# Kernel optimization log

Hardware: AMD Instinct MI355X
Metric: run time of the kernel (lower is better)

## Reference

```python
import jax, jax.numpy as jnp
import numpy as np

N = 8192
F_IN = 128
F_OUT = 128
NEG_SLOPE = 0.2


def setup_inputs() -> dict:
    key = jax.random.key(0)
    k_h, k_adj, k_W, k_a = jax.random.split(key, 4)
    h = jax.random.normal(k_h, (N, F_IN), dtype=jnp.float32)
    # binary adjacency mask as float (the module multiplies scores by adj)
    adj = (jax.random.uniform(k_adj, (N, N)) < 0.05).astype(jnp.float32)
    # nn.Linear(in, out, bias=False): weight shape [out, in]
    W = jax.random.normal(k_W, (F_OUT, F_IN), dtype=jnp.float32) / np.sqrt(F_IN)
    # nn.Linear(2*out, 1, bias=False): weight shape [1, 2*out]
    a = jax.random.normal(k_a, (1, 2 * F_OUT), dtype=jnp.float32) / np.sqrt(2 * F_OUT)
    return {"h": h, "adj": adj, "W": W, "a": a}


def reference(h, adj, W, a):
    # Wh: [N, F_out]
    Wh = h @ W.T
    f = Wh.shape[-1]
    # a([Wh_i ; Wh_j]) factored: e[i, j] = leaky_relu(Wh[i]@a1 + Wh[j]@a2)
    a1 = a[0, :f]  # [F_out]
    a2 = a[0, f:]  # [F_out]
    s_i = Wh @ a1  # [N]
    s_j = Wh @ a2  # [N]
    e = jax.nn.leaky_relu(s_i[:, None] + s_j[None, :], NEG_SLOPE)  # [N, N]
    # faithful to original: softmax over dim=1 of e * adj (multiplicative mask)
    attention = jax.nn.softmax(e * adj, axis=1)  # [N, N]
    return attention @ Wh  # [N, F_out]
```

## Files before the change

kernel.cpp:

```cpp
#include <hip/hip_runtime.h>

#define N_NODES 8192
#define FDIM 128
#define NEG_SLOPE 0.2f
#define SEG 512

__device__ __forceinline__ unsigned int f2bf(float f) {
  unsigned int u = __float_as_uint(f);
  return (u + 0x7FFFu + ((u >> 16) & 1u)) >> 16;
}

__global__ __launch_bounds__(256) void transpose_w_kernel(
    const float* __restrict__ W, float* __restrict__ WtG) {
  int idx = blockIdx.x * 256 + threadIdx.x;
  WtG[idx] = W[(idx & 127) * FDIM + (idx >> 7)];
}

__global__ __launch_bounds__(256) void wh_fused_kernel(
    const float* __restrict__ h, const float* __restrict__ WtG,
    const float* __restrict__ a,
    unsigned int* __restrict__ Whb,
    float* __restrict__ s1, float* __restrict__ s2,
    float* __restrict__ S) {
  __shared__ float Wt[FDIM * 132];
  __shared__ float rows[32 * 132];
  const int t = threadIdx.x;
  const int base = blockIdx.x * 32;
  for (int it = 0; it < 16; ++it) {
    int idx = t + 256 * it;
    int k = idx >> 5, c = (idx & 31) * 4;
    *(float4*)&Wt[k * 132 + c] = *(const float4*)&WtG[k * FDIM + c];
  }
  for (int it = 0; it < 4; ++it) {
    int idx = t + 256 * it;
    int r = idx >> 5, c = (idx & 31) * 4;
    *(float4*)&rows[r * 132 + c] =
        *(const float4*)&h[(size_t)(base + r) * FDIM + c];
  }
  __syncthreads();
  const int c4 = (t & 31) * 4;
  const int g = t >> 5;
  float acc[4][4];
#pragma unroll
  for (int rr = 0; rr < 4; ++rr)
#pragma unroll
    for (int cc = 0; cc < 4; ++cc) acc[rr][cc] = 0.f;
  for (int k = 0; k < FDIM; ++k) {
    float4 wv = *(const float4*)&Wt[k * 132 + c4];
    float rv[4];
#pragma unroll
    for (int rr = 0; rr < 4; ++rr) rv[rr] = rows[(4 * g + rr) * 132 + k];
#pragma unroll
    for (int rr = 0; rr < 4; ++rr) {
      acc[rr][0] += rv[rr] * wv.x;
      acc[rr][1] += rv[rr] * wv.y;
      acc[rr][2] += rv[rr] * wv.z;
      acc[rr][3] += rv[rr] * wv.w;
    }
  }
#pragma unroll
  for (int rr = 0; rr < 4; ++rr) {
    int r = base + 4 * g + rr;
    unsigned int p0 = f2bf(acc[rr][0]) | (f2bf(acc[rr][1]) << 16);
    unsigned int p1 = f2bf(acc[rr][2]) | (f2bf(acc[rr][3]) << 16);
    *(uint2*)&Whb[(size_t)r * 64 + (c4 >> 1)] = make_uint2(p0, p1);
  }
  {
    float4 a1v = *(const float4*)&a[c4];
    float4 a2v = *(const float4*)&a[FDIM + c4];
#pragma unroll
    for (int rr = 0; rr < 4; ++rr) {
      float d1 = acc[rr][0] * a1v.x + acc[rr][1] * a1v.y +
                 acc[rr][2] * a1v.z + acc[rr][3] * a1v.w;
      float d2 = acc[rr][0] * a2v.x + acc[rr][1] * a2v.y +
                 acc[rr][2] * a2v.z + acc[rr][3] * a2v.w;
#pragma unroll
      for (int off = 16; off; off >>= 1) {
        d1 += __shfl_down(d1, off);
        d2 += __shfl_down(d2, off);
      }
      if ((t & 31) == 0) {
        s1[base + 4 * g + rr] = d1;
        s2[base + 4 * g + rr] = d2;
      }
    }
  }
  __syncthreads();
  float4 cs = make_float4(acc[0][0] + acc[1][0] + acc[2][0] + acc[3][0],
                          acc[0][1] + acc[1][1] + acc[2][1] + acc[3][1],
                          acc[0][2] + acc[1][2] + acc[2][2] + acc[3][2],
                          acc[0][3] + acc[1][3] + acc[2][3] + acc[3][3]);
  *(float4*)&rows[g * FDIM + c4] = cs;
  __syncthreads();
  if (t < FDIM) {
    float s = 0.f;
#pragma unroll
    for (int gg = 0; gg < 8; ++gg) s += rows[gg * FDIM + t];
    atomicAdd(&S[t], s);
  }
}

__device__ __forceinline__ float4 ntload4(const float4* p) {
  typedef float f4v __attribute__((ext_vector_type(4)));
  f4v v = __builtin_nontemporal_load((const f4v*)p);
  return make_float4(v[0], v[1], v[2], v[3]);
}

__device__ __forceinline__ int mbcnt64(unsigned long long b) {
  return (int)__builtin_amdgcn_mbcnt_hi(
      (unsigned)(b >> 32), __builtin_amdgcn_mbcnt_lo((unsigned)b, 0u));
}

__global__ __launch_bounds__(256, 4) void gat_row_kernel(
    const float* __restrict__ adj, const unsigned int* __restrict__ Whb,
    const float* __restrict__ s1, const float* __restrict__ s2,
    const float* __restrict__ S, float* __restrict__ out) {
  const int i = blockIdx.x;
  const int t = threadIdx.x;
  const int lane = t & 63;
  const int wave = t >> 6;
  __shared__ float2 pairs[4 * SEG];
  __shared__ int counts[4];
  __shared__ float red[4];
  __shared__ float red2[4];
  __shared__ float fpart[4][FDIM];

  const float s1i = s1[i];
  const float4* __restrict__ arow = (const float4*)(adj + (size_t)i * N_NODES);
  const float4* __restrict__ srow = (const float4*)s2;
  float2* __restrict__ mypairs = pairs + wave * SEG;

  float4 av[8], sv[8];
#pragma unroll
  for (int it = 0; it < 8; ++it) av[it] = ntload4(&arow[it * 256 + t]);
#pragma unroll
  for (int it = 0; it < 8; ++it) sv[it] = srow[it * 256 + t];
  int cbase = 0;
  float lmax = -1e30f;
#pragma unroll
  for (int it = 0; it < 8; ++it) {
    const int j4 = it * 256 + t;
    float vv[4] = {av[it].x, av[it].y, av[it].z, av[it].w};
    float ss[4] = {sv[it].x, sv[it].y, sv[it].z, sv[it].w};
#pragma unroll
    for (int c = 0; c < 4; ++c) {
      bool pred = (vv[c] != 0.f);
      float e = s1i + ss[c];
      e = e > 0.f ? e : NEG_SLOPE * e;
      unsigned long long b = __ballot(pred);
      if (pred) {
        int pos = cbase + mbcnt64(b);
        if (pos < SEG) {
          float2 pr;
          pr.x = e;
          ((int*)&pr)[1] = j4 * 4 + c;
          mypairs[pos] = pr;
        }
      }
      lmax = fmaxf(lmax, pred ? e : -1e30f);
      cbase += (int)__popcll(b);
    }
  }
  const int mycnt = cbase < SEG ? cbase : SEG;
  if (lane == 0) counts[wave] = mycnt;
  for (int off = 32; off; off >>= 1) lmax = fmaxf(lmax, __shfl_down(lmax, off));
  if (lane == 0) red[wave] = lmax;
  __syncthreads();
  const int cnt = counts[0] + counts[1] + counts[2] + counts[3];
  float m = fmaxf(fmaxf(red[0], red[1]), fmaxf(red[2], red[3]));
  if (cnt < N_NODES) m = fmaxf(m, 0.f);
  const float em = __expf(-m);

  const int half = lane >> 5, lq = lane & 31;
  const uint2* __restrict__ Whb2 = (const uint2*)Whb;
  float ax = 0.f, ay = 0.f, az = 0.f, aw = 0.f, lsum = 0.f;
  const int nit = (mycnt + 1) >> 1;
  int it = 0;
  for (; it + 3 < nit; it += 4) {
#pragma unroll
    for (int c = 0; c < 4; ++c) {
      int p = 2 * (it + c) + half;
      bool ok = p < mycnt;
      float2 pr = mypairs[ok ? p : 0];
      int j = ((const int*)&pr)[1];
      uint2 d = Whb2[((size_t)j << 5) + lq];
      float pv = __expf(pr.x - m);
      float w = ok ? pv - em : 0.f;
      lsum += ok ? pv : 0.f;
      ax += w * __uint_as_float(d.x << 16);
      ay += w * __uint_as_float(d.x & 0xffff0000u);
      az += w * __uint_as_float(d.y << 16);
      aw += w * __uint_as_float(d.y & 0xffff0000u);
    }
  }
  for (; it < nit; ++it) {
    int p = 2 * it + half;
    bool ok = p < mycnt;
    float2 pr = mypairs[ok ? p : 0];
    int j = ((const int*)&pr)[1];
    uint2 d = Whb2[((size_t)j << 5) + lq];
    float pv = __expf(pr.x - m);
    float w = ok ? pv - em : 0.f;
    lsum += ok ? pv : 0.f;
    ax += w * __uint_as_float(d.x << 16);
    ay += w * __uint_as_float(d.x & 0xffff0000u);
    az += w * __uint_as_float(d.y << 16);
    aw += w * __uint_as_float(d.y & 0xffff0000u);
  }
  for (int off = 32; off; off >>= 1) lsum += __shfl_down(lsum, off);
  if (lane == 0) red2[wave] = lsum * (1.f / 32.f);
  ax += __shfl_down(ax, 32);
  ay += __shfl_down(ay, 32);
  az += __shfl_down(az, 32);
  aw += __shfl_down(aw, 32);
  if (lane < 32)
    *(float4*)&fpart[wave][4 * lq] = make_float4(ax, ay, az, aw);
  __syncthreads();
  if (t < FDIM) {
    float l = red2[0] + red2[1] + red2[2] + red2[3]
              + (float)(N_NODES - cnt) * em;
    float o = (fpart[0][t] + fpart[1][t] + fpart[2][t] + fpart[3][t]
               + em * S[t]) / l;
    out[(size_t)i * FDIM + t] = o;
  }
}

extern "C" void kernel_launch(void* const* d_in, const int* in_sizes, int n_in,
                              void* d_out, int out_size, void* d_ws, size_t ws_size,
                              hipStream_t stream) {
  const float* h   = (const float*)d_in[0];
  const float* adj = (const float*)d_in[1];
  const float* W   = (const float*)d_in[2];
  const float* a   = (const float*)d_in[3];
  float* out = (float*)d_out;
  unsigned int* Whb = (unsigned int*)d_ws;
  float* s1  = (float*)(Whb + (size_t)N_NODES * 64);
  float* s2  = s1 + N_NODES;
  float* S   = s2 + N_NODES;
  float* WtG = S + FDIM;

  hipMemsetAsync(S, 0, FDIM * sizeof(float), stream);
  hipLaunchKernelGGL(transpose_w_kernel, dim3(FDIM * FDIM / 256), dim3(256), 0,
                     stream, W, WtG);
  hipLaunchKernelGGL(wh_fused_kernel, dim3(N_NODES / 32), dim3(256), 0, stream,
                     h, WtG, a, Whb, s1, s2, S);
  hipLaunchKernelGGL(gat_row_kernel, dim3(N_NODES), dim3(256), 0, stream,
                     adj, Whb, s1, s2, S, out);
}
```

Before: 410.2 us.

## Split row kernel into separate adjacency scan and sparse gather kernels

The fused per-row kernel is split into a scan kernel, which streams the adjacency row and writes compacted (score, index) pairs plus per-wave counts and maxima to global workspace, and a gather kernel, which reads those pairs and accumulates bf16 Wh rows. The gather now loads 16-byte vectors per lane, with four neighbours per wave step instead of two. The aim is to keep the bandwidth-bound scan from being stalled by latency-bound gathers and to let each phase run at its own occupancy. The cost is a global round trip for the pair lists (about 128 MB written and read) and an extra launch.

Measured after the change: 458.6 us. +11.8%, slower.

```diff
diff --git a/kernel.cpp b/kernel.cpp
--- a/kernel.cpp
+++ b/kernel.cpp
@@ -111,24 +111,17 @@
       (unsigned)(b >> 32), __builtin_amdgcn_mbcnt_lo((unsigned)b, 0u));
 }
 
-__global__ __launch_bounds__(256, 4) void gat_row_kernel(
-    const float* __restrict__ adj, const unsigned int* __restrict__ Whb,
-    const float* __restrict__ s1, const float* __restrict__ s2,
-    const float* __restrict__ S, float* __restrict__ out) {
+__global__ __launch_bounds__(256, 4) void scan_kernel(
+    const float* __restrict__ adj, const float* __restrict__ s1,
+    const float* __restrict__ s2, float2* __restrict__ pairs,
+    int* __restrict__ cnt4, float* __restrict__ wmax) {
   const int i = blockIdx.x;
   const int t = threadIdx.x;
-  const int lane = t & 63;
-  const int wave = t >> 6;
-  __shared__ float2 pairs[4 * SEG];
-  __shared__ int counts[4];
-  __shared__ float red[4];
-  __shared__ float red2[4];
-  __shared__ float fpart[4][FDIM];
-
+  const int lane = t & 63, wave = t >> 6;
   const float s1i = s1[i];
   const float4* __restrict__ arow = (const float4*)(adj + (size_t)i * N_NODES);
   const float4* __restrict__ srow = (const float4*)s2;
-  float2* __restrict__ mypairs = pairs + wave * SEG;
+  float2* __restrict__ mypairs = pairs + (size_t)i * (4 * SEG) + wave * SEG;
 
   float4 av[8], sv[8];
 #pragma unroll
@@ -162,59 +155,68 @@
     }
   }
   const int mycnt = cbase < SEG ? cbase : SEG;
-  if (lane == 0) counts[wave] = mycnt;
   for (int off = 32; off; off >>= 1) lmax = fmaxf(lmax, __shfl_down(lmax, off));
-  if (lane == 0) red[wave] = lmax;
-  __syncthreads();
-  const int cnt = counts[0] + counts[1] + counts[2] + counts[3];
-  float m = fmaxf(fmaxf(red[0], red[1]), fmaxf(red[2], red[3]));
+  if (lane == 0) {
+    cnt4[4 * i + wave] = mycnt;
+    wmax[4 * i + wave] = lmax;
+  }
+}
+
+__global__ __launch_bounds__(256, 4) void gather_kernel(
+    const unsigned int* __restrict__ Whb, const float2* __restrict__ pairs,
+    const int* __restrict__ cnt4, const float* __restrict__ wmax,
+    const float* __restrict__ S, float* __restrict__ out) {
+  const int i = blockIdx.x;
+  const int t = threadIdx.x;
+  const int lane = t & 63, wave = t >> 6;
+  __shared__ float fpart[4][FDIM];
+  __shared__ float red2[4];
+
+  const int4 cc = *(const int4*)&cnt4[4 * i];
+  const float4 wm = *(const float4*)&wmax[4 * i];
+  const int cnt = cc.x + cc.y + cc.z + cc.w;
+  const int mycnt = wave == 0 ? cc.x : wave == 1 ? cc.y : wave == 2 ? cc.z : cc.w;
+  float m = fmaxf(fmaxf(wm.x, wm.y), fmaxf(wm.z, wm.w));
   if (cnt < N_NODES) m = fmaxf(m, 0.f);
   const float em = __expf(-m);
 
-  const int half = lane >> 5, lq = lane & 31;
-  const uint2* __restrict__ Whb2 = (const uint2*)Whb;
-  float ax = 0.f, ay = 0.f, az = 0.f, aw = 0.f, lsum = 0.f;
-  const int nit = (mycnt + 1) >> 1;
-  int it = 0;
-  for (; it + 3 < nit; it += 4) {
-#pragma unroll
-    for (int c = 0; c < 4; ++c) {
-      int p = 2 * (it + c) + half;
-      bool ok = p < mycnt;
-      float2 pr = mypairs[ok ? p : 0];
-      int j = ((const int*)&pr)[1];
-      uint2 d = Whb2[((size_t)j << 5) + lq];
-      float pv = __expf(pr.x - m);
-      float w = ok ? pv - em : 0.f;
-      lsum += ok ? pv : 0.f;
-      ax += w * __uint_as_float(d.x << 16);
-      ay += w * __uint_as_float(d.x & 0xffff0000u);
-      az += w * __uint_as_float(d.y << 16);
-      aw += w * __uint_as_float(d.y & 0xffff0000u);
-    }
-  }
-  for (; it < nit; ++it) {
-    int p = 2 * it + half;
+  const float2* __restrict__ mypairs = pairs + (size_t)i * (4 * SEG) + wave * SEG;
+  const int q = lane >> 4, lq = lane & 15;
+  const uint4* __restrict__ Whb4 = (const uint4*)Whb;
+  float acc[8];
+#pragma unroll
+  for (int e = 0; e < 8; ++e) acc[e] = 0.f;
+  float lsum = 0.f;
+  const int nit = (mycnt + 3) >> 2;
+  for (int it = 0; it < nit; ++it) {
+    int p = 4 * it + q;
     bool ok = p < mycnt;
     float2 pr = mypairs[ok ? p : 0];
-    int j = ((const int*)&pr)[1];
-    uint2 d = Whb2[((size_t)j << 5) + lq];
+    int j = ((const int*)&pr)[1] & (N_NODES - 1);
+    uint4 d = Whb4[((size_t)j << 4) + lq];
     float pv = __expf(pr.x - m);
     float w = ok ? pv - em : 0.f;
     lsum += ok ? pv : 0.f;
-    ax += w * __uint_as_float(d.x << 16);
-    ay += w * __uint_as_float(d.x & 0xffff0000u);
-    az += w * __uint_as_float(d.y << 16);
-    aw += w * __uint_as_float(d.y & 0xffff0000u);
+    acc[0] += w * __uint_as_float(d.x << 16);
+    acc[1] += w * __uint_as_float(d.x & 0xffff0000u);
+    acc[2] += w * __uint_as_float(d.y << 16);
+    acc[3] += w * __uint_as_float(d.y & 0xffff0000u);
+    acc[4] += w * __uint_as_float(d.z << 16);
+    acc[5] += w * __uint_as_float(d.z & 0xffff0000u);
+    acc[6] += w * __uint_as_float(d.w << 16);
+    acc[7] += w * __uint_as_float(d.w & 0xffff0000u);
   }
   for (int off = 32; off; off >>= 1) lsum += __shfl_down(lsum, off);
-  if (lane == 0) red2[wave] = lsum * (1.f / 32.f);
-  ax += __shfl_down(ax, 32);
-  ay += __shfl_down(ay, 32);
-  az += __shfl_down(az, 32);
-  aw += __shfl_down(aw, 32);
-  if (lane < 32)
-    *(float4*)&fpart[wave][4 * lq] = make_float4(ax, ay, az, aw);
+  if (lane == 0) red2[wave] = lsum * (1.f / 16.f);
+#pragma unroll
+  for (int e = 0; e < 8; ++e) {
+    acc[e] += __shfl_down(acc[e], 32);
+    acc[e] += __shfl_down(acc[e], 16);
+  }
+  if (lane < 16) {
+    *(float4*)&fpart[wave][lq * 8] = make_float4(acc[0], acc[1], acc[2], acc[3]);
+    *(float4*)&fpart[wave][lq * 8 + 4] = make_float4(acc[4], acc[5], acc[6], acc[7]);
+  }
   __syncthreads();
   if (t < FDIM) {
     float l = red2[0] + red2[1] + red2[2] + red2[3]
@@ -234,16 +236,21 @@
   const float* a   = (const float*)d_in[3];
   float* out = (float*)d_out;
   unsigned int* Whb = (unsigned int*)d_ws;
-  float* s1  = (float*)(Whb + (size_t)N_NODES * 64);
-  float* s2  = s1 + N_NODES;
-  float* S   = s2 + N_NODES;
-  float* WtG = S + FDIM;
+  float* s1   = (float*)(Whb + (size_t)N_NODES * 64);
+  float* s2   = s1 + N_NODES;
+  float* S    = s2 + N_NODES;
+  float* WtG  = S + FDIM;
+  int*   cnt4 = (int*)(WtG + FDIM * FDIM);
+  float* wmax = (float*)(cnt4 + 4 * N_NODES);
+  float2* pairs = (float2*)(wmax + 4 * N_NODES);
 
   hipMemsetAsync(S, 0, FDIM * sizeof(float), stream);
   hipLaunchKernelGGL(transpose_w_kernel, dim3(FDIM * FDIM / 256), dim3(256), 0,
                      stream, W, WtG);
   hipLaunchKernelGGL(wh_fused_kernel, dim3(N_NODES / 32), dim3(256), 0, stream,
                      h, WtG, a, Whb, s1, s2, S);
-  hipLaunchKernelGGL(gat_row_kernel, dim3(N_NODES), dim3(256), 0, stream,
-                     adj, Whb, s1, s2, S, out);
-}
+  hipLaunchKernelGGL(scan_kernel, dim3(N_NODES), dim3(256), 0, stream,
+                     adj, s1, s2, pairs, cnt4, wmax);
+  hipLaunchKernelGGL(gather_kernel, dim3(N_NODES), dim3(256), 0, stream,
+                     Whb, pairs, cnt4, wmax, S, out);
+}
```

## Process four rows per block with double-buffered adjacency prefetch and wider Wh gathers

Applied to the files above, without the earlier changes.

Each block now handles four consecutive rows and issues the nontemporal adjacency loads for the next row before the current row's sync and gather phase, so the memory stream overlaps with compute. The gather phase switches from 64-bit loads over two half-waves to 128-bit loads, with four lanes groups of 16 per wave each covering one neighbour. The aim is to hide adjacency-load latency and reduce gather instructions, at the cost of more registers for the double buffer, fewer blocks, and an extra shuffle stage in the reduction. Loop-carried dependencies between rows and the shared-memory reuse across rows are guarded by the existing syncs.

Result: no change. 417.2 us (+1.7%).

```diff
diff --git a/kernel.cpp b/kernel.cpp
--- a/kernel.cpp
+++ b/kernel.cpp
@@ -4,6 +4,7 @@
 #define FDIM 128
 #define NEG_SLOPE 0.2f
 #define SEG 512
+#define ROWS 4
 
 __device__ __forceinline__ unsigned int f2bf(float f) {
   unsigned int u = __float_as_uint(f);
@@ -111,118 +112,128 @@
       (unsigned)(b >> 32), __builtin_amdgcn_mbcnt_lo((unsigned)b, 0u));
 }
 
-__global__ __launch_bounds__(256, 4) void gat_row_kernel(
+__global__ __launch_bounds__(256, 4) void gat_pipe_kernel(
     const float* __restrict__ adj, const unsigned int* __restrict__ Whb,
     const float* __restrict__ s1, const float* __restrict__ s2,
     const float* __restrict__ S, float* __restrict__ out) {
-  const int i = blockIdx.x;
   const int t = threadIdx.x;
-  const int lane = t & 63;
-  const int wave = t >> 6;
+  const int lane = t & 63, wave = t >> 6;
   __shared__ float2 pairs[4 * SEG];
   __shared__ int counts[4];
   __shared__ float red[4];
   __shared__ float red2[4];
   __shared__ float fpart[4][FDIM];
-
-  const float s1i = s1[i];
-  const float4* __restrict__ arow = (const float4*)(adj + (size_t)i * N_NODES);
+  float2* __restrict__ mypairs = pairs + wave * SEG;
   const float4* __restrict__ srow = (const float4*)s2;
-  float2* __restrict__ mypairs = pairs + wave * SEG;
-
-  float4 av[8], sv[8];
-#pragma unroll
-  for (int it = 0; it < 8; ++it) av[it] = ntload4(&arow[it * 256 + t]);
-#pragma unroll
-  for (int it = 0; it < 8; ++it) sv[it] = srow[it * 256 + t];
-  int cbase = 0;
-  float lmax = -1e30f;
-#pragma unroll
-  for (int it = 0; it < 8; ++it) {
-    const int j4 = it * 256 + t;
-    float vv[4] = {av[it].x, av[it].y, av[it].z, av[it].w};
-    float ss[4] = {sv[it].x, sv[it].y, sv[it].z, sv[it].w};
-#pragma unroll
-    for (int c = 0; c < 4; ++c) {
-      bool pred = (vv[c] != 0.f);
-      float e = s1i + ss[c];
-      e = e > 0.f ? e : NEG_SLOPE * e;
-      unsigned long long b = __ballot(pred);
-      if (pred) {
-        int pos = cbase + mbcnt64(b);
-        if (pos < SEG) {
-          float2 pr;
-          pr.x = e;
-          ((int*)&pr)[1] = j4 * 4 + c;
-          mypairs[pos] = pr;
-        }
-      }
-      lmax = fmaxf(lmax, pred ? e : -1e30f);
-      cbase += (int)__popcll(b);
-    }
-  }
-  const int mycnt = cbase < SEG ? cbase : SEG;
-  if (lane == 0) counts[wave] = mycnt;
-  for (int off = 32; off; off >>= 1) lmax = fmaxf(lmax, __shfl_down(lmax, off));
-  if (lane == 0) red[wave] = lmax;
-  __syncthreads();
-  const int cnt = counts[0] + counts[1] + counts[2] + counts[3];
-  float m = fmaxf(fmaxf(red[0], red[1]), fmaxf(red[2], red[3]));
-  if (cnt < N_NODES) m = fmaxf(m, 0.f);
-  const float em = __expf(-m);
-
-  const int half = lane >> 5, lq = lane & 31;
-  const uint2* __restrict__ Whb2 = (const uint2*)Whb;
-  float ax = 0.f, ay = 0.f, az = 0.f, aw = 0.f, lsum = 0.f;
-  const int nit = (mycnt + 1) >> 1;
-  int it = 0;
-  for (; it + 3 < nit; it += 4) {
-#pragma unroll
-    for (int c = 0; c < 4; ++c) {
-      int p = 2 * (it + c) + half;
-      bool ok = p < mycnt;
-      float2 pr = mypairs[ok ? p : 0];
-      int j = ((const int*)&pr)[1];
-      uint2 d = Whb2[((size_t)j << 5) + lq];
-      float pv = __expf(pr.x - m);
-      float w = ok ? pv - em : 0.f;
-      lsum += ok ? pv : 0.f;
-      ax += w * __uint_as_float(d.x << 16);
-      ay += w * __uint_as_float(d.x & 0xffff0000u);
-      az += w * __uint_as_float(d.y << 16);
-      aw += w * __uint_as_float(d.y & 0xffff0000u);
-    }
-  }
-  for (; it < nit; ++it) {
-    int p = 2 * it + half;
-    bool ok = p < mycnt;
-    float2 pr = mypairs[ok ? p : 0];
-    int j = ((const int*)&pr)[1];
-    uint2 d = Whb2[((size_t)j << 5) + lq];
-    float pv = __expf(pr.x - m);
-    float w = ok ? pv - em : 0.f;
-    lsum += ok ? pv : 0.f;
-    ax += w * __uint_as_float(d.x << 16);
-    ay += w * __uint_as_float(d.x & 0xffff0000u);
-    az += w * __uint_as_float(d.y << 16);
-    aw += w * __uint_as_float(d.y & 0xffff0000u);
-  }
-  for (int off = 32; off; off >>= 1) lsum += __shfl_down(lsum, off);
-  if (lane == 0) red2[wave] = lsum * (1.f / 32.f);
-  ax += __shfl_down(ax, 32);
-  ay += __shfl_down(ay, 32);
-  az += __shfl_down(az, 32);
-  aw += __shfl_down(aw, 32);
-  if (lane < 32)
-    *(float4*)&fpart[wave][4 * lq] = make_float4(ax, ay, az, aw);
-  __syncthreads();
-  if (t < FDIM) {
-    float l = red2[0] + red2[1] + red2[2] + red2[3]
-              + (float)(N_NODES - cnt) * em;
-    float o = (fpart[0][t] + fpart[1][t] + fpart[2][t] + fpart[3][t]
-               + em * S[t]) / l;
-    out[(size_t)i * FDIM + t] = o;
-  }
+  const uint4* __restrict__ Whb4 = (const uint4*)Whb;
+  const int q = lane >> 4, lq = lane & 15;
+
+  const int base = blockIdx.x * ROWS;
+  const float4 s1v = *(const float4*)&s1[base];
+
+  float4 a0[8], a1[8];
+#define ISSUE(BUF, ROW)                                                     \
+  {                                                                         \
+    const float4* __restrict__ ar =                                         \
+        (const float4*)(adj + (size_t)(ROW)*N_NODES);                       \
+    _Pragma("unroll") for (int it = 0; it < 8; ++it)                        \
+        BUF[it] = ntload4(&ar[it * 256 + t]);                               \
+  }
+
+#define PROC(AV, RR, DO_NEXT, NEXTBUF)                                      \
+  {                                                                         \
+    const int i = base + (RR);                                              \
+    const float s1i = ((const float*)&s1v)[RR];                             \
+    int cbase = 0;                                                          \
+    float lmax = -1e30f;                                                    \
+    _Pragma("unroll") for (int it = 0; it < 8; ++it) {                      \
+      const int j4 = it * 256 + t;                                          \
+      float4 svv = srow[it * 256 + t];     \
+      float vv[4] = {AV[it].x, AV[it].y, AV[it].z, AV[it].w};               \
+      float ss[4] = {svv.x, svv.y, svv.z, svv.w};                           \
+      _Pragma("unroll") for (int c = 0; c < 4; ++c) {                       \
+        bool pred = (vv[c] != 0.f);                                         \
+        float e = s1i + ss[c];                                              \
+        e = e > 0.f ? e : NEG_SLOPE * e;                                    \
+        unsigned long long b = __ballot(pred);                              \
+        if (pred) {                                                         \
+          int pos = cbase + mbcnt64(b);                                     \
+          if (pos < SEG) {                                                  \
+            float2 pr;                                                      \
+            pr.x = e;                                                       \
+            ((int*)&pr)[1] = j4 * 4 + c;                                    \
+            mypairs[pos] = pr;                                              \
+          }                                                                 \
+        }                                                                   \
+        lmax = fmaxf(lmax, pred ? e : -1e30f);                              \
+        cbase += (int)__popcll(b);                                          \
+      }                                                                     \
+    }                                                                       \
+    const int mycnt = cbase < SEG ? cbase : SEG;                            \
+    if (lane == 0) counts[wave] = mycnt;                                    \
+    for (int off = 32; off; off >>= 1)                                      \
+      lmax = fmaxf(lmax, __shfl_down(lmax, off));                           \
+    if (lane == 0) red[wave] = lmax;                                        \
+    if (DO_NEXT) ISSUE(NEXTBUF, base + (RR) + 1);    \
+    __syncthreads();                                                        \
+    const int cnt = counts[0] + counts[1] + counts[2] + counts[3];          \
+    float m = fmaxf(fmaxf(red[0], red[1]), fmaxf(red[2], red[3]));          \
+    if (cnt < N_NODES) m = fmaxf(m, 0.f);                                   \
+    const float em = __expf(-m);                                            \
+    float acc0 = 0.f, acc1 = 0.f, acc2 = 0.f, acc3 = 0.f;                   \
+    float acc4 = 0.f, acc5 = 0.f, acc6 = 0.f, acc7 = 0.f;                   \
+    float lsum = 0.f;                                                       \
+    const int nit = (mycnt + 3) >> 2;                                       \
+    for (int itg = 0; itg < nit; ++itg) {                                   \
+      int p = 4 * itg + q;                                                  \
+      bool ok = p < mycnt;                                                  \
+      float2 pr = mypairs[ok ? p : 0];                                      \
+      int j = ((const int*)&pr)[1] & (N_NODES - 1);                         \
+      uint4 d = Whb4[((size_t)j << 4) + lq];                                \
+      float pv = __expf(pr.x - m);                                          \
+      float w = ok ? pv - em : 0.f;                                         \
+      lsum += ok ? pv : 0.f;                                                \
+      acc0 += w * __uint_as_float(d.x << 16);                               \
+      acc1 += w * __uint_as_float(d.x & 0xffff0000u);                       \
+      acc2 += w * __uint_as_float(d.y << 16);                               \
+      acc3 += w * __uint_as_float(d.y & 0xffff0000u);                       \
+      acc4 += w * __uint_as_float(d.z << 16);                               \
+      acc5 += w * __uint_as_float(d.z & 0xffff0000u);                       \
+      acc6 += w * __uint_as_float(d.w << 16);                               \
+      acc7 += w * __uint_as_float(d.w & 0xffff0000u);                       \
+    }                                                                       \
+    for (int off = 32; off; off >>= 1) lsum += __shfl_down(lsum, off);      \
+    if (lane == 0) red2[wave] = lsum * (1.f / 16.f);                        \
+    acc0 += __shfl_down(acc0, 32); acc0 += __shfl_down(acc0, 16);           \
+    acc1 += __shfl_down(acc1, 32); acc1 += __shfl_down(acc1, 16);           \
+    acc2 += __shfl_down(acc2, 32); acc2 += __shfl_down(acc2, 16);           \
+    acc3 += __shfl_down(acc3, 32); acc3 += __shfl_down(acc3, 16);           \
+    acc4 += __shfl_down(acc4, 32); acc4 += __shfl_down(acc4, 16);           \
+    acc5 += __shfl_down(acc5, 32); acc5 += __shfl_down(acc5, 16);           \
+    acc6 += __shfl_down(acc6, 32); acc6 += __shfl_down(acc6, 16);           \
+    acc7 += __shfl_down(acc7, 32); acc7 += __shfl_down(acc7, 16);           \
+    if (lane < 16) {                                                        \
+      *(float4*)&fpart[wave][lq * 8] = make_float4(acc0, acc1, acc2, acc3); \
+      *(float4*)&fpart[wave][lq * 8 + 4] =                                  \
+          make_float4(acc4, acc5, acc6, acc7);                              \
+    }                                                                       \
+    __syncthreads();                                                        \
+    if (t < FDIM) {                                                         \
+      float l = red2[0] + red2[1] + red2[2] + red2[3] +                     \
+                (float)(N_NODES - cnt) * em;                                \
+      float o = (fpart[0][t] + fpart[1][t] + fpart[2][t] + fpart[3][t] +    \
+                 em * S[t]) / l;                                            \
+      out[(size_t)i * FDIM + t] = o;                                        \
+    }                                                                       \
+  }
+
+  ISSUE(a0, base);
+  PROC(a0, 0, 1, a1);
+  PROC(a1, 1, 1, a0);
+  PROC(a0, 2, 1, a1);
+  PROC(a1, 3, 0, a0);
+#undef PROC
+#undef ISSUE
 }
 
 extern "C" void kernel_launch(void* const* d_in, const int* in_sizes, int n_in,
@@ -244,6 +255,6 @@
                      stream, W, WtG);
   hipLaunchKernelGGL(wh_fused_kernel, dim3(N_NODES / 32), dim3(256), 0, stream,
                      h, WtG, a, Whb, s1, s2, S);
-  hipLaunchKernelGGL(gat_row_kernel, dim3(N_NODES), dim3(256), 0, stream,
-                     adj, Whb, s1, s2, S, out);
-}
+  hipLaunchKernelGGL(gat_pipe_kernel, dim3(N_NODES / ROWS), dim3(256), 0,
+                     stream, adj, Whb, s1, s2, S, out);
+}
```
